# Optimization experiments

Hardware: AMD Instinct MI355X
Metric: run time of the kernel (lower is better)

## Reference

```python
import jax, jax.numpy as jnp
import numpy as np

B, L, S, D, H, CTX = 2, 2048, 512, 1024, 16, 1024
HD = D // H
HID = 4 * D
EPS = 1e-6


def _ln(x):
    mu = jnp.mean(x, axis=-1, keepdims=True)
    var = jnp.mean((x - mu) ** 2, axis=-1, keepdims=True)
    return (x - mu) * jax.lax.rsqrt(var + EPS)


def _rotate_half(x):
    x1, x2 = jnp.split(x, 2, axis=-1)
    return jnp.concatenate([-x2, x1], axis=-1)


def _heads(t):  # [B,N,D] -> [B,H,N,HD]
    return t.reshape(t.shape[0], t.shape[1], H, HD).transpose(0, 2, 1, 3)


def _merge(t):  # [B,H,N,HD] -> [B,N,D]
    return t.transpose(0, 2, 1, 3).reshape(t.shape[0], t.shape[2], D)


def setup_inputs() -> dict:
    key = jax.random.key(0)
    ks = jax.random.split(key, 24)
    s = 0.02
    inp = {
        "x": jax.random.normal(ks[0], (B, L, D), jnp.float32),
        "timestep_emb": jax.random.normal(ks[1], (B, D), jnp.float32),
        "context_emb": jax.random.normal(ks[2], (B, S, CTX), jnp.float32),
        "rope_emb": jax.random.normal(ks[3], (L, HD), jnp.float32),
        # adaLN modulation: Linear(D -> 6D) with bias
        "w_mod": jax.random.normal(ks[4], (D, 6 * D), jnp.float32) * s,
        "b_mod": jnp.zeros((6 * D,), jnp.float32),
        # self-attention (no qkv bias, out has bias)
        "wq_s": jax.random.normal(ks[5], (D, D), jnp.float32) * s,
        "wk_s": jax.random.normal(ks[6], (D, D), jnp.float32) * s,
        "wv_s": jax.random.normal(ks[7], (D, D), jnp.float32) * s,
        "wo_s": jax.random.normal(ks[8], (D, D), jnp.float32) * s,
        "bo_s": jnp.zeros((D,), jnp.float32),
        # cross-attention (q/k/v no bias, out has bias)
        "wq_c": jax.random.normal(ks[9], (D, D), jnp.float32) * s,
        "wk_c": jax.random.normal(ks[10], (CTX, D), jnp.float32) * s,
        "wv_c": jax.random.normal(ks[11], (CTX, D), jnp.float32) * s,
        "wo_c": jax.random.normal(ks[12], (D, D), jnp.float32) * s,
        "bo_c": jnp.zeros((D,), jnp.float32),
        # MLP
        "w1": jax.random.normal(ks[13], (D, HID), jnp.float32) * s,
        "b1": jnp.zeros((HID,), jnp.float32),
        "w2": jax.random.normal(ks[14], (HID, D), jnp.float32) * s,
        "b2": jnp.zeros((D,), jnp.float32),
    }
    return inp


def reference(x, timestep_emb, context_emb, rope_emb,
              w_mod, b_mod,
              wq_s, wk_s, wv_s, wo_s, bo_s,
              wq_c, wk_c, wv_c, wo_c, bo_c,
              w1, b1, w2, b2):
    scale = HD ** -0.5
    # adaLN modulation from timestep embedding
    mods = jnp.split(timestep_emb @ w_mod + b_mod, 6, axis=-1)
    shift_msa, scale_msa, gate_msa, shift_mlp, scale_mlp, gate_mlp = mods

    # --- self-attention with RoPE ---
    nx = _ln(x) * (1.0 + scale_msa[:, None, :]) + shift_msa[:, None, :]
    q = _heads(nx @ wq_s)
    k = _heads(nx @ wk_s)
    v = _heads(nx @ wv_s)
    cos = jnp.cos(rope_emb)[None, None]  # [1,1,L,HD]
    sin = jnp.sin(rope_emb)[None, None]
    q = q * cos + _rotate_half(q) * sin
    k = k * cos + _rotate_half(k) * sin
    attn = jax.nn.softmax(jnp.einsum("bhqd,bhkd->bhqk", q, k) * scale, axis=-1)
    sa = _merge(jnp.einsum("bhqk,bhkd->bhqd", attn, v)) @ wo_s + bo_s
    x = x + gate_msa[:, None, :] * sa

    # --- cross-attention (no mask) ---
    nx = _ln(x)
    q = _heads(nx @ wq_c)
    k = _heads(context_emb @ wk_c)
    v = _heads(context_emb @ wv_c)
    attn = jax.nn.softmax(jnp.einsum("bhqd,bhkd->bhqk", q, k) * scale, axis=-1)
    ca = _merge(jnp.einsum("bhqk,bhkd->bhqd", attn, v)) @ wo_c + bo_c
    x = x + ca

    # --- MLP with modulation + gate ---
    nx = _ln(x) * (1.0 + scale_mlp[:, None, :]) + shift_mlp[:, None, :]
    h = jax.nn.gelu(nx @ w1 + b1, approximate=False)
    x = x + gate_mlp[:, None, :] * (h @ w2 + b2)
    return x
```

## Files before the change

kernel.cpp:

```cpp
#include <hip/hip_runtime.h>
#include <hip/hip_bf16.h>


typedef short short8 __attribute__((ext_vector_type(8)));
typedef float f32x4 __attribute__((ext_vector_type(4)));
typedef float f32x16 __attribute__((ext_vector_type(16)));

#define DEV __device__ __forceinline__

DEV unsigned short f2b(float f) {
  __hip_bfloat16 h = __float2bfloat16(f);
  return *reinterpret_cast<unsigned short*>(&h);
}
DEV float b2f(unsigned short u) {
  unsigned int x = ((unsigned int)u) << 16;
  return __builtin_bit_cast(float, x);
}
DEV unsigned int pk2(float lo, float hi) {
  unsigned int r;
  asm("v_cvt_pk_bf16_f32 %0, %1, %2" : "=v"(r) : "v"(lo), "v"(hi));
  return r;
}
DEV void vpsw(unsigned int& a, unsigned int& b) {
  asm("v_permlane32_swap_b32 %0, %1" : "+v"(a), "+v"(b));
}
DEV float max3f(float a, float b, float c) {
  float r;
  asm("v_max3_f32 %0, %1, %2, %3" : "=v"(r) : "v"(a), "v"(b), "v"(c));
  return r;
}

#define GLB(p) ((const __attribute__((address_space(1))) void*)(p))
#define LDSP(p) ((__attribute__((address_space(3))) void*)(p))

struct TCB { const float* in; unsigned short* out; float scale; };
struct PrepArgs {
  const float* wmod; unsigned short* wmodT;
  TCB sq[8];
  const float* w1; unsigned short* w1T;
  const float* w2; unsigned short* w2T;
  const float* ctx; unsigned short* ctxb;
  const float* rope; float2* cs;
};

__global__ __launch_bounds__(256) void prep(PrepArgs a) {
  __shared__ float t32[32][33];
  const int blk = blockIdx.x;
  const int tx = threadIdx.x & 31, ty = threadIdx.x >> 5;
  if (blk < 22528) {
    const float* in;
    unsigned short* out;
    int R, C, gx, tile;
    float scale;
    if (blk < 6144) {
      in = a.wmod; out = a.wmodT; R = 1024; C = 6144; gx = 192; tile = blk; scale = 1.f;
    } else if (blk < 14336) {
      int j = (blk - 6144) >> 10;
      tile = (blk - 6144) & 1023;
      in = a.sq[j].in; out = a.sq[j].out; scale = a.sq[j].scale;
      R = 1024; C = 1024; gx = 32;
    } else if (blk < 18432) {
      tile = blk - 14336;
      in = a.w1; out = a.w1T; R = 1024; C = 4096; gx = 128; scale = 1.f;
    } else {
      tile = blk - 18432;
      in = a.w2; out = a.w2T; R = 4096; C = 1024; gx = 32; scale = 1.f;
    }
    int bx = (tile % gx) * 32, by = (tile / gx) * 32;
#pragma unroll
    for (int i = ty; i < 32; i += 8)
      t32[i][tx] = in[(size_t)(by + i) * C + bx + tx];
    __syncthreads();
#pragma unroll
    for (int i = ty; i < 32; i += 8)
      out[(size_t)(bx + i) * R + by + tx] = f2b(t32[tx][i] * scale);
  } else if (blk < 26624) {
    int i = (blk - 22528) * 256 + threadIdx.x;
    a.ctxb[i] = f2b(a.ctx[i]);
  } else {
    int i = (blk - 26624) * 256 + threadIdx.x;
    float v = a.rope[i];
    a.cs[i] = make_float2(cosf(v), sinf(v));
  }
}

__global__ __launch_bounds__(256) void mods_kernel(
    const float* __restrict__ te, const unsigned short* __restrict__ wmodT,
    const float* __restrict__ bmod, float* __restrict__ mods) {
  int w = blockIdx.x * 4 + (threadIdx.x >> 6);
  int lane = threadIdx.x & 63;
  int b = w / 6144, j = w % 6144;
  const unsigned short* wr = wmodT + (size_t)j * 1024;
  const float* ter = te + (size_t)b * 1024;
  int k0 = lane * 16;
  float sum = 0.f;
#pragma unroll
  for (int u = 0; u < 2; ++u) {
    short8 wv = *(const short8*)(wr + k0 + u * 8);
#pragma unroll
    for (int e = 0; e < 8; ++e)
      sum += b2f((unsigned short)wv[e]) * ter[k0 + u * 8 + e];
  }
#pragma unroll
  for (int off = 32; off >= 1; off >>= 1) sum += __shfl_down(sum, off);
  if (lane == 0) mods[(size_t)b * 6144 + j] = sum + bmod[j];
}

__global__ __launch_bounds__(256) void ln_mod(
    const float* __restrict__ x, const float* __restrict__ mods,
    unsigned short* __restrict__ out, int scale_ofs, int shift_ofs) {
  int row = blockIdx.x;
  int b = row >> 11;
  int tid = threadIdx.x;
  const float* xr = x + (size_t)row * 1024;
  float4 v = ((const float4*)xr)[tid];
  float s = v.x + v.y + v.z + v.w;
  float ss = v.x * v.x + v.y * v.y + v.z * v.z + v.w * v.w;
#pragma unroll
  for (int off = 32; off >= 1; off >>= 1) {
    s += __shfl_down(s, off);
    ss += __shfl_down(ss, off);
  }
  __shared__ float red[8];
  int wave = tid >> 6, lane = tid & 63;
  if (lane == 0) { red[wave] = s; red[4 + wave] = ss; }
  __syncthreads();
  if (tid == 0) {
    float S = red[0] + red[1] + red[2] + red[3];
    float SS = red[4] + red[5] + red[6] + red[7];
    float mu = S * (1.f / 1024.f);
    red[0] = mu;
    red[1] = SS * (1.f / 1024.f) - mu * mu;
  }
  __syncthreads();
  float mu = red[0];
  float rs = rsqrtf(red[1] + 1e-6f);
  float vv[4] = {v.x, v.y, v.z, v.w};
  unsigned short o[4];
#pragma unroll
  for (int c = 0; c < 4; ++c) {
    int col = tid * 4 + c;
    float nv = (vv[c] - mu) * rs;
    if (scale_ofs >= 0)
      nv = nv * (1.f + mods[(size_t)b * 6144 + scale_ofs + col]) +
           mods[(size_t)b * 6144 + shift_ofs + col];
    o[c] = f2b(nv);
  }
  *(ushort4*)(&out[(size_t)row * 1024 + tid * 4]) = *(const ushort4*)o;
}

template <int EPI, int MI, int NJ>
DEV void gemm_epilogue(f32x4 (&acc)[MI][NJ], void* Cout, const float* bias,
                       const float* mods, int gate_ofs, const float* src,
                       int N, int rowsPerB, int m0, int n0, int wm, int wn,
                       int g, int r) {
#pragma unroll
  for (int i = 0; i < MI; ++i) {
#pragma unroll
    for (int j = 0; j < NJ; ++j) {
#pragma unroll
      for (int q = 0; q < 4; ++q) {
        size_t grow = (size_t)(m0 + wm + i * 16 + g * 4 + q);
        size_t gcol = (size_t)(n0 + wn + j * 16 + r);
        float v = acc[i][j][q];
        if constexpr (EPI == 0) {
          ((unsigned short*)Cout)[grow * N + gcol] = f2b(v);
        } else if constexpr (EPI == 1) {
          v += bias[gcol];
          float ge = 0.5f * v * (1.0f + erff(v * 0.70710678f));
          ((unsigned short*)Cout)[grow * N + gcol] = f2b(ge);
        } else if constexpr (EPI == 3) {
          size_t buf = gcol >> 10;
          ((unsigned short*)Cout)[buf * (4096ull * 1024) + grow * 1024 + (gcol & 1023)] = f2b(v);
        } else {
          v += bias[gcol];
          float gate = 1.0f;
          if (gate_ofs >= 0)
            gate = mods[(grow / rowsPerB) * 6144 + gate_ofs + gcol];
          ((float*)Cout)[grow * N + gcol] = src[grow * N + gcol] + gate * v;
        }
      }
    }
  }
}

DEV void qkv_rope_epilogue(f32x4 (&acc)[4][4], unsigned short* Cout,
                           const float2* cs, int m0, int n0, int wm, int wn,
                           int g, int r) {
  const int buf = (n0 + wn) >> 10;
  const int colbase = (n0 + wn) & 1023;
  unsigned short* base = Cout + (size_t)buf * (4096ull * 1024);
#pragma unroll
  for (int i = 0; i < 4; ++i) {
#pragma unroll
    for (int q = 0; q < 4; ++q) {
      size_t grow = (size_t)(m0 + wm + i * 16 + g * 4 + q);
      unsigned short* orow = base + grow * 1024 + colbase + r;
      if (buf < 2) {
        int l = (int)(grow & 2047);
#pragma unroll
        for (int j = 0; j < 2; ++j) {
          int d = j * 16 + r;
          float2 a = cs[l * 64 + d];
          float2 bb = cs[l * 64 + d + 32];
          float x1 = acc[i][j][q], x2 = acc[i][j + 2][q];
          orow[j * 16] = f2b(x1 * a.x - x2 * a.y);
          orow[(j + 2) * 16] = f2b(x2 * bb.x + x1 * bb.y);
        }
      } else {
#pragma unroll
        for (int j = 0; j < 4; ++j) orow[j * 16] = f2b(acc[i][j][q]);
      }
    }
  }
}

template <int EPI>
__global__ __launch_bounds__(256, 2) void gemm_bt(
    const unsigned short* __restrict__ A, const unsigned short* __restrict__ Bt,
    void* __restrict__ Cout, const float* __restrict__ bias,
    const float* __restrict__ mods, int gate_ofs, const float* __restrict__ src,
    int M, int N, int K, int rowsPerB) {
  __shared__ unsigned short As[128 * 32];
  __shared__ unsigned short Bs[128 * 32];
  const int tid = threadIdx.x;
  const int wave = tid >> 6, lane = tid & 63;
  const int g = lane >> 4, r = lane & 15;
  const int m0 = blockIdx.y * 128, n0 = blockIdx.x * 128;
  const int wm = (wave >> 1) * 64, wn = (wave & 1) * 64;
  const int srow = lane >> 2;
  const int scol = (lane & 3) * 8;

  f32x4 acc[4][4] = {};

  for (int k0 = 0; k0 < K; k0 += 32) {
    __syncthreads();
#pragma unroll
    for (int cc = 0; cc < 4; ++cc) {
      int c = wave * 4 + cc;
      int isB = c >> 3;
      int cl = c & 7;
      int row = cl * 16 + srow;
      const unsigned short* gsrc =
          isB ? (Bt + (size_t)(n0 + row) * K + k0 + scol)
              : (A + (size_t)(m0 + row) * K + k0 + scol);
      unsigned short* ldst = (isB ? Bs : As) + cl * 512;
      __builtin_amdgcn_global_load_lds(GLB(gsrc), LDSP(ldst), 16, 0, 0);
    }
    __syncthreads();

    short8 bfr[4];
#pragma unroll
    for (int j = 0; j < 4; ++j)
      bfr[j] = *(const short8*)(&Bs[(wn + j * 16 + r) * 32 + g * 8]);
#pragma unroll
    for (int i = 0; i < 4; ++i) {
      short8 af = *(const short8*)(&As[(wm + i * 16 + r) * 32 + g * 8]);
#pragma unroll
      for (int j = 0; j < 4; ++j)
        acc[i][j] = __builtin_amdgcn_mfma_f32_16x16x32_bf16(af, bfr[j], acc[i][j], 0, 0, 0);
    }
  }
  gemm_epilogue<EPI, 4, 4>(acc, Cout, bias, mods, gate_ofs, src, N, rowsPerB,
                           m0, n0, wm, wn, g, r);
}

template <int EPI>
__global__ __launch_bounds__(256) void gemm_pipe(
    const unsigned short* __restrict__ A, const unsigned short* __restrict__ Bt,
    void* __restrict__ Cout, const float* __restrict__ bias,
    const float* __restrict__ mods, int gate_ofs, const float* __restrict__ src,
    int M, int N, int K, int rowsPerB, int mshift) {
  __shared__ unsigned short lds[4 * 16384];
  const int tid = threadIdx.x;
  const int wave = tid >> 6, lane = tid & 63;
  const int g = lane >> 4, r = lane & 15;
  const int flat = blockIdx.x;
  const int xcd = flat & 7, idx = flat >> 3;
  const int mt = xcd * (1 << mshift) + (idx & ((1 << mshift) - 1));
  const int nt = idx >> mshift;
  const int m0 = mt * 128, n0 = nt * 128;
  const int wm = (wave >> 1) * 64, wn = (wave & 1) * 64;
  const int srow8 = lane >> 3;
  const int sck = (lane & 7) ^ srow8;

  f32x4 acc[4][4] = {};

  auto stage = [&](int t, int bufi) {
    const int k0 = t * 64;
#pragma unroll
    for (int i = 0; i < 8; ++i) {
      int u = wave * 8 + i;
      int isB = u >> 4;
      int uu = u & 15;
      int rl = uu * 8 + srow8;
      const unsigned short* gsrc =
          (isB ? (Bt + (size_t)(n0 + rl) * K) : (A + (size_t)(m0 + rl) * K)) +
          k0 + sck * 8;
      unsigned short* dst = (unsigned short*)lds + bufi * 16384 + isB * 8192 + uu * 512;
      __builtin_amdgcn_global_load_lds(GLB(gsrc), LDSP(dst), 16, 0, 0);
    }
  };

  const int nt_k = K / 64;
  stage(0, 0);
  stage(1, 1);
  stage(2, 2);

  for (int t = 0; t < nt_k; ++t) {
    int rem = nt_k - t;
    if (rem >= 3) {
      asm volatile("s_waitcnt vmcnt(16)" ::: "memory");
    } else if (rem == 2) {
      asm volatile("s_waitcnt vmcnt(8)" ::: "memory");
    } else {
      asm volatile("s_waitcnt vmcnt(0)" ::: "memory");
    }
    __builtin_amdgcn_sched_barrier(0);
    __builtin_amdgcn_s_barrier();
    __builtin_amdgcn_sched_barrier(0);
    if (t + 3 < nt_k) stage(t + 3, (t + 3) & 3);

    const unsigned short* Ab = (const unsigned short*)lds + (t & 3) * 16384;
    const unsigned short* Bb = Ab + 8192;
#pragma unroll
    for (int ks = 0; ks < 2; ++ks) {
      short8 bfr[4];
#pragma unroll
      for (int j = 0; j < 4; ++j) {
        int row = wn + j * 16 + r;
        bfr[j] = *(const short8*)&Bb[row * 64 + ((g + ks * 4) ^ (r & 7)) * 8];
      }
#pragma unroll
      for (int i = 0; i < 4; ++i) {
        int row = wm + i * 16 + r;
        short8 af = *(const short8*)&Ab[row * 64 + ((g + ks * 4) ^ (r & 7)) * 8];
#pragma unroll
        for (int j = 0; j < 4; ++j)
          acc[i][j] = __builtin_amdgcn_mfma_f32_16x16x32_bf16(af, bfr[j], acc[i][j], 0, 0, 0);
      }
    }
  }
  if constexpr (EPI == 4) {
    qkv_rope_epilogue(acc, (unsigned short*)Cout, (const float2*)bias,
                      m0, n0, wm, wn, g, r);
  } else {
    gemm_epilogue<EPI, 4, 4>(acc, Cout, bias, mods, gate_ofs, src, N, rowsPerB,
                             m0, n0, wm, wn, g, r);
  }
}

template <int EPI>
__global__ __launch_bounds__(256) void gemm_p2(
    const unsigned short* __restrict__ A, const unsigned short* __restrict__ Bt,
    void* __restrict__ Cout, const float* __restrict__ bias,
    const float* __restrict__ mods, int gate_ofs, const float* __restrict__ src,
    int M, int N, int K, int rowsPerB, int ntn) {
  __shared__ unsigned short lds[3 * 12288];
  const int tid = threadIdx.x;
  const int wave = tid >> 6, lane = tid & 63;
  const int g = lane >> 4, r = lane & 15;
  const int flat = blockIdx.x;
  const int nt = flat % ntn, mt = flat / ntn;
  const int m0 = mt * 64, n0 = nt * 128;
  const int wm = (wave >> 1) * 32, wn = (wave & 1) * 64;
  const int srow8 = lane >> 3;
  const int sck = (lane & 7) ^ srow8;

  f32x4 acc[2][4] = {};

  auto stage = [&](int t, int bufi) {
    const int k0 = t * 64;
    unsigned short* base = (unsigned short*)lds + bufi * 12288;
#pragma unroll
    for (int i = 0; i < 2; ++i) {
      int u = wave * 2 + i;
      int rl = u * 8 + srow8;
      const unsigned short* gsrc = A + (size_t)(m0 + rl) * K + k0 + sck * 8;
      __builtin_amdgcn_global_load_lds(GLB(gsrc), LDSP(base + u * 512), 16, 0, 0);
    }
#pragma unroll
    for (int i = 0; i < 4; ++i) {
      int u = wave * 4 + i;
      int rl = u * 8 + srow8;
      const unsigned short* gsrc = Bt + (size_t)(n0 + rl) * K + k0 + sck * 8;
      __builtin_amdgcn_global_load_lds(GLB(gsrc), LDSP(base + 4096 + u * 512), 16, 0, 0);
    }
  };

  const int ntk = K / 64;
  stage(0, 0);
  stage(1, 1);
  int cbuf = 0, sbuf = 2;

  for (int t = 0; t < ntk; ++t) {
    if (t < ntk - 1) {
      asm volatile("s_waitcnt vmcnt(6)" ::: "memory");
    } else {
      asm volatile("s_waitcnt vmcnt(0)" ::: "memory");
    }
    __builtin_amdgcn_sched_barrier(0);
    __builtin_amdgcn_s_barrier();
    __builtin_amdgcn_sched_barrier(0);
    if (t + 2 < ntk) {
      stage(t + 2, sbuf);
      sbuf = (sbuf == 2) ? 0 : sbuf + 1;
    }

    const unsigned short* Ab = (const unsigned short*)lds + cbuf * 12288;
    const unsigned short* Bb = Ab + 4096;
#pragma unroll
    for (int ks = 0; ks < 2; ++ks) {
      short8 bfr[4];
#pragma unroll
      for (int j = 0; j < 4; ++j) {
        int row = wn + j * 16 + r;
        bfr[j] = *(const short8*)&Bb[row * 64 + ((g + ks * 4) ^ (r & 7)) * 8];
      }
#pragma unroll
      for (int i = 0; i < 2; ++i) {
        int row = wm + i * 16 + r;
        short8 af = *(const short8*)&Ab[row * 64 + ((g + ks * 4) ^ (r & 7)) * 8];
#pragma unroll
        for (int j = 0; j < 4; ++j)
          acc[i][j] = __builtin_amdgcn_mfma_f32_16x16x32_bf16(af, bfr[j], acc[i][j], 0, 0, 0);
      }
    }
    cbuf = (cbuf == 2) ? 0 : cbuf + 1;
  }
  gemm_epilogue<EPI, 2, 4>(acc, Cout, bias, mods, gate_ofs, src, N, rowsPerB,
                           m0, n0, wm, wn, g, r);
}

__global__ __launch_bounds__(256) void gemm_cross(
    const unsigned short* __restrict__ Anx, const unsigned short* __restrict__ Bq,
    unsigned short* __restrict__ Oq,
    const unsigned short* __restrict__ Actx, const unsigned short* __restrict__ Bkv,
    unsigned short* __restrict__ Okv) {
  __shared__ unsigned short lds[3 * 12288];
  const int tid = threadIdx.x;
  const int wave = tid >> 6, lane = tid & 63;
  const int g = lane >> 4, r = lane & 15;
  const bool iskv = blockIdx.x >= 512;
  const int flat = iskv ? (blockIdx.x - 512) : blockIdx.x;
  const int ntn = iskv ? 16 : 8;
  const unsigned short* A = iskv ? Actx : Anx;
  const unsigned short* Bt = iskv ? Bkv : Bq;
  const int nt = flat % ntn, mt = flat / ntn;
  const int m0 = mt * 64, n0 = nt * 128;
  const int K = 1024;
  const int wm = (wave >> 1) * 32, wn = (wave & 1) * 64;
  const int srow8 = lane >> 3;
  const int sck = (lane & 7) ^ srow8;

  f32x4 acc[2][4] = {};

  auto stage = [&](int t, int bufi) {
    const int k0 = t * 64;
    unsigned short* base = (unsigned short*)lds + bufi * 12288;
#pragma unroll
    for (int i = 0; i < 2; ++i) {
      int u = wave * 2 + i;
      int rl = u * 8 + srow8;
      const unsigned short* gsrc = A + (size_t)(m0 + rl) * K + k0 + sck * 8;
      __builtin_amdgcn_global_load_lds(GLB(gsrc), LDSP(base + u * 512), 16, 0, 0);
    }
#pragma unroll
    for (int i = 0; i < 4; ++i) {
      int u = wave * 4 + i;
      int rl = u * 8 + srow8;
      const unsigned short* gsrc = Bt + (size_t)(n0 + rl) * K + k0 + sck * 8;
      __builtin_amdgcn_global_load_lds(GLB(gsrc), LDSP(base + 4096 + u * 512), 16, 0, 0);
    }
  };

  const int ntk = K / 64;
  stage(0, 0);
  stage(1, 1);
  int cbuf = 0, sbuf = 2;

  for (int t = 0; t < ntk; ++t) {
    if (t < ntk - 1) {
      asm volatile("s_waitcnt vmcnt(6)" ::: "memory");
    } else {
      asm volatile("s_waitcnt vmcnt(0)" ::: "memory");
    }
    __builtin_amdgcn_sched_barrier(0);
    __builtin_amdgcn_s_barrier();
    __builtin_amdgcn_sched_barrier(0);
    if (t + 2 < ntk) {
      stage(t + 2, sbuf);
      sbuf = (sbuf == 2) ? 0 : sbuf + 1;
    }

    const unsigned short* Ab = (const unsigned short*)lds + cbuf * 12288;
    const unsigned short* Bb = Ab + 4096;
#pragma unroll
    for (int ks = 0; ks < 2; ++ks) {
      short8 bfr[4];
#pragma unroll
      for (int j = 0; j < 4; ++j) {
        int row = wn + j * 16 + r;
        bfr[j] = *(const short8*)&Bb[row * 64 + ((g + ks * 4) ^ (r & 7)) * 8];
      }
#pragma unroll
      for (int i = 0; i < 2; ++i) {
        int row = wm + i * 16 + r;
        short8 af = *(const short8*)&Ab[row * 64 + ((g + ks * 4) ^ (r & 7)) * 8];
#pragma unroll
        for (int j = 0; j < 4; ++j)
          acc[i][j] = __builtin_amdgcn_mfma_f32_16x16x32_bf16(af, bfr[j], acc[i][j], 0, 0, 0);
      }
    }
    cbuf = (cbuf == 2) ? 0 : cbuf + 1;
  }

#pragma unroll
  for (int i = 0; i < 2; ++i) {
#pragma unroll
    for (int j = 0; j < 4; ++j) {
#pragma unroll
      for (int q = 0; q < 4; ++q) {
        size_t grow = (size_t)(m0 + wm + i * 16 + g * 4 + q);
        size_t gcol = (size_t)(n0 + wn + j * 16 + r);
        float v = acc[i][j][q];
        if (iskv) {
          size_t buf = gcol >> 10;
          Okv[buf * (4096ull * 1024) + grow * 1024 + (gcol & 1023)] = f2b(v);
        } else {
          Oq[grow * 1024 + gcol] = f2b(v);
        }
      }
    }
  }
}

__global__ __launch_bounds__(256, 2) void flash2(
    const unsigned short* __restrict__ Q, const unsigned short* __restrict__ Kv,
    const unsigned short* __restrict__ Vv, unsigned short* __restrict__ O,
    int Lk) {
  __shared__ unsigned short lds[20480];
  const int tid = threadIdx.x, wave = tid >> 6, lane = tid & 63;
  const int hi = lane >> 5, lq = lane & 31;
  const int flat = blockIdx.x;
  const int xcd = flat & 7, rr = flat >> 3;
  const int gl = rr >> 4, qt = rr & 15;
  const int g = xcd * 4 + gl;
  const int h = g & 15, b = g >> 4;
  const int Lq = 2048, D = 1024;

  const unsigned short* Qbase =
      Q + ((size_t)b * Lq + qt * 128 + wave * 32 + lq) * D + h * 64;
  const unsigned short* Kbase = Kv + (size_t)b * Lk * D + h * 64;
  const unsigned short* Vbase = Vv + (size_t)b * Lk * D + h * 64;

  short8 qf[4];
#pragma unroll
  for (int kb = 0; kb < 4; ++kb)
    qf[kb] = *(const short8*)(Qbase + kb * 16 + hi * 8);

  const short8 ones = {0x3F80, 0x3F80, 0x3F80, 0x3F80, 0x3F80, 0x3F80, 0x3F80, 0x3F80};
  const f32x16 z16 = {};

  const int kr0 = tid >> 3, kc0 = tid & 7;
  const int kvp = tid >> 3, db = tid & 7;
  const int kch0 = (kc0 ^ (kr0 & 7) ^ (kr0 >> 3)) & 7;
  const int kch1 = kch0 ^ 4;
  const int f0 = (lq & 7) ^ (lq >> 3);
  const int swz0 = f0 << 4, swz1 = swz0 ^ 64;

  int vby[8];
#pragma unroll
  for (int e = 0; e < 8; ++e) {
    int d = db * 8 + e;
    vby[e] = d * 128 + ((kvp * 4) ^ (((e ^ db) & 7) << 4));
  }

  float m_run = -3.0e38f;
  f32x16 o0 = {}, o1 = {}, lacc = {};
  short8 vr0, vr1;
  short8 pbf[4];

  auto stageK = [&](int t, int bi) {
    const unsigned short* s0 = Kbase + (size_t)(t * 64 + kr0) * D + kch0 * 8;
    const unsigned short* s1 = Kbase + (size_t)(t * 64 + kr0 + 32) * D + kch1 * 8;
    __builtin_amdgcn_global_load_lds(GLB(s0), LDSP(&lds[bi * 4096 + wave * 512]), 16, 0, 0);
    __builtin_amdgcn_global_load_lds(GLB(s1), LDSP(&lds[bi * 4096 + 2048 + wave * 512]), 16, 0, 0);
  };
  auto loadV = [&](int t) {
    const unsigned short* v0 = Vbase + (size_t)(t * 64 + 2 * kvp) * D + db * 8;
    vr0 = *(const short8*)v0;
    vr1 = *(const short8*)(v0 + D);
  };
  auto writeV = [&](int t) {
    char* vt = (char*)&lds[12288 + (t & 1) * 4096];
    union { short8 s; unsigned int u[4]; } a, c;
    a.s = vr0; c.s = vr1;
#pragma unroll
    for (int k = 0; k < 4; ++k) {
      *(unsigned int*)(vt + vby[2 * k]) =
          __builtin_amdgcn_perm(c.u[k], a.u[k], 0x05040100u);
      *(unsigned int*)(vt + vby[2 * k + 1]) =
          __builtin_amdgcn_perm(c.u[k], a.u[k], 0x07060302u);
    }
  };
  auto qk = [&](int bi, f32x16& sa0, f32x16& sa1) {
    const unsigned short* K0 = &lds[bi * 4096];
    {
      int lo = hi * 16;
      short8 a0 = *(const short8*)&K0[lq * 64 + ((lo ^ swz0) >> 1)];
      short8 a1 = *(const short8*)&K0[(32 + lq) * 64 + ((lo ^ swz1) >> 1)];
      sa0 = __builtin_amdgcn_mfma_f32_32x32x16_bf16(a0, qf[0], z16, 0, 0, 0);
      sa1 = __builtin_amdgcn_mfma_f32_32x32x16_bf16(a1, qf[0], z16, 0, 0, 0);
    }
#pragma unroll
    for (int ks = 1; ks < 4; ++ks) {
      int lo = ks * 32 + hi * 16;
      short8 a0 = *(const short8*)&K0[lq * 64 + ((lo ^ swz0) >> 1)];
      short8 a1 = *(const short8*)&K0[(32 + lq) * 64 + ((lo ^ swz1) >> 1)];
      sa0 = __builtin_amdgcn_mfma_f32_32x32x16_bf16(a0, qf[ks], sa0, 0, 0, 0);
      sa1 = __builtin_amdgcn_mfma_f32_32x32x16_bf16(a1, qf[ks], sa1, 0, 0, 0);
    }
  };
  auto finish = [&](f32x16& s0a, f32x16& s1a) {
    float tm[8];
#pragma unroll
    for (int i = 0; i < 8; ++i)
      tm[i] = fmaxf(max3f(s0a[i], s0a[i + 8], s1a[i]), s1a[i + 8]);
    float x = max3f(tm[0], tm[1], tm[2]);
    float y = max3f(tm[3], tm[4], tm[5]);
    float pm = fmaxf(max3f(tm[6], tm[7], x), y);
    {
      unsigned int ua = __builtin_bit_cast(unsigned int, pm), ub = ua;
      vpsw(ua, ub);
      pm = fmaxf(__builtin_bit_cast(float, ua), __builtin_bit_cast(float, ub));
    }
    if (__any(pm - m_run > 8.0f)) {
      float mnew = fmaxf(m_run, pm);
      float alpha = exp2f(m_run - mnew);
      lacc[0] *= alpha;
#pragma unroll
      for (int i = 0; i < 16; ++i) { o0[i] *= alpha; o1[i] *= alpha; }
      m_run = mnew;
    }
    float mc = m_run;
#pragma unroll
    for (int i = 0; i < 16; ++i) s0a[i] = exp2f(s0a[i] - mc);
#pragma unroll
    for (int i = 0; i < 16; ++i) s1a[i] = exp2f(s1a[i] - mc);
#pragma unroll
    for (int kb = 0; kb < 4; ++kb) {
      int bb = (kb & 1) * 8;
      float p0, p1, p2, p3, p4, p5, p6, p7;
      if (kb < 2) {
        p0 = s0a[bb + 0]; p1 = s0a[bb + 1]; p2 = s0a[bb + 2]; p3 = s0a[bb + 3];
        p4 = s0a[bb + 4]; p5 = s0a[bb + 5]; p6 = s0a[bb + 6]; p7 = s0a[bb + 7];
      } else {
        p0 = s1a[bb + 0]; p1 = s1a[bb + 1]; p2 = s1a[bb + 2]; p3 = s1a[bb + 3];
        p4 = s1a[bb + 4]; p5 = s1a[bb + 5]; p6 = s1a[bb + 6]; p7 = s1a[bb + 7];
      }
      unsigned int u0 = pk2(p0, p1), u1 = pk2(p2, p3);
      unsigned int u2 = pk2(p4, p5), u3 = pk2(p6, p7);
      vpsw(u0, u2);
      vpsw(u1, u3);
      union { unsigned int u[4]; short8 s; } fr;
      fr.u[0] = u0; fr.u[1] = u1; fr.u[2] = u2; fr.u[3] = u3;
      pbf[kb] = fr.s;
    }
  };
  auto pv = [&](int t) {
    const unsigned short* V0 = &lds[12288 + (t & 1) * 4096];
    __builtin_amdgcn_s_setprio(1);
#pragma unroll
    for (int kb = 0; kb < 4; ++kb) {
      int lo = kb * 32 + hi * 16;
      short8 vf0 = *(const short8*)&V0[lq * 64 + ((lo ^ swz0) >> 1)];
      short8 vf1 = *(const short8*)&V0[(32 + lq) * 64 + ((lo ^ swz1) >> 1)];
      o0 = __builtin_amdgcn_mfma_f32_32x32x16_bf16(vf0, pbf[kb], o0, 0, 0, 0);
      o1 = __builtin_amdgcn_mfma_f32_32x32x16_bf16(vf1, pbf[kb], o1, 0, 0, 0);
      lacc = __builtin_amdgcn_mfma_f32_32x32x16_bf16(ones, pbf[kb], lacc, 0, 0, 0);
    }
    __builtin_amdgcn_s_setprio(0);
  };

  const int nkt = Lk / 64;

  stageK(0, 0);
  loadV(0);
  writeV(0);
  stageK(1, 1);
  __syncthreads();

  f32x16 sA0, sA1, sB0, sB1;
  qk(0, sA0, sA1);

  auto pstep = [&](int t, f32x16& n0, f32x16& n1, f32x16& p0, f32x16& p1) {
    const int tq = t + 1;
    if (tq < nkt) {
      loadV(tq);
      if (tq + 1 < nkt) stageK(tq + 1, (tq + 1) % 3);
      qk(tq % 3, n0, n1);
    }
    finish(p0, p1);
    if (tq < nkt) writeV(tq);
    pv(t);
    __syncthreads();
  };

  for (int t = 0; t < nkt; t += 2) {
    pstep(t, sB0, sB1, sA0, sA1);
    pstep(t + 1, sA0, sA1, sB0, sB1);
  }

  float rl = 1.0f / lacc[0];
  unsigned short* os = &lds[wave * 2048];
#pragma unroll
  for (int t = 0; t < 2; ++t) {
#pragma unroll
    for (int c = 0; c < 4; ++c) {
      int dbase = 32 * t + 8 * c + 4 * hi;
      float v0 = (t ? o1[4 * c + 0] : o0[4 * c + 0]) * rl;
      float v1 = (t ? o1[4 * c + 1] : o0[4 * c + 1]) * rl;
      float v2 = (t ? o1[4 * c + 2] : o0[4 * c + 2]) * rl;
      float v3 = (t ? o1[4 * c + 3] : o0[4 * c + 3]) * rl;
      int by0 = lq * 128 + ((dbase * 2) ^ ((lq & 7) << 4));
      int by1 = lq * 128 + (((dbase + 2) * 2) ^ ((lq & 7) << 4));
      *(unsigned int*)((char*)os + by0) = pk2(v0, v1);
      *(unsigned int*)((char*)os + by1) = pk2(v2, v3);
    }
  }
  int q2 = lane >> 1;
  unsigned short* orow =
      O + ((size_t)b * Lq + qt * 128 + wave * 32 + q2) * D + h * 64;
#pragma unroll
  for (int j = 0; j < 4; ++j) {
    int j2 = (lane & 1) * 4 + j;
    int byr = q2 * 128 + ((j2 * 16) ^ ((q2 & 7) << 4));
    short8 vv = *(const short8*)((char*)os + byr);
    *(short8*)(orow + j2 * 8) = vv;
  }
}

extern "C" void kernel_launch(void* const* d_in, const int* in_sizes, int n_in,
                              void* d_out, int out_size, void* d_ws, size_t ws_size,
                              hipStream_t stream) {
  (void)in_sizes; (void)n_in; (void)out_size; (void)ws_size;
  const float* x_in = (const float*)d_in[0];
  const float* te   = (const float*)d_in[1];
  const float* ctx  = (const float*)d_in[2];
  const float* rope = (const float*)d_in[3];
  const float* wmod = (const float*)d_in[4];
  const float* bmod = (const float*)d_in[5];
  const float* wqs  = (const float*)d_in[6];
  const float* wks  = (const float*)d_in[7];
  const float* wvs  = (const float*)d_in[8];
  const float* wos  = (const float*)d_in[9];
  const float* bos  = (const float*)d_in[10];
  const float* wqc  = (const float*)d_in[11];
  const float* wkc  = (const float*)d_in[12];
  const float* wvc  = (const float*)d_in[13];
  const float* woc  = (const float*)d_in[14];
  const float* boc  = (const float*)d_in[15];
  const float* w1   = (const float*)d_in[16];
  const float* b1   = (const float*)d_in[17];
  const float* w2   = (const float*)d_in[18];
  const float* b2   = (const float*)d_in[19];
  float* out = (float*)d_out;

  char* w = (char*)d_ws;
  size_t o = 0;
  auto alloc = [&](size_t bytes) {
    char* p = w + o;
    o = (o + bytes + 255) & ~(size_t)255;
    return p;
  };
  unsigned short* wmodT = (unsigned short*)alloc(6144ull * 1024 * 2);
  unsigned short* wqsT  = (unsigned short*)alloc(1024ull * 1024 * 2);
  unsigned short* wksT  = (unsigned short*)alloc(1024ull * 1024 * 2);
  unsigned short* wvsT  = (unsigned short*)alloc(1024ull * 1024 * 2);
  unsigned short* wosT  = (unsigned short*)alloc(1024ull * 1024 * 2);
  unsigned short* wqcT  = (unsigned short*)alloc(1024ull * 1024 * 2);
  unsigned short* wkcT  = (unsigned short*)alloc(1024ull * 1024 * 2);
  unsigned short* wvcT  = (unsigned short*)alloc(1024ull * 1024 * 2);
  unsigned short* wocT  = (unsigned short*)alloc(1024ull * 1024 * 2);
  unsigned short* w1T   = (unsigned short*)alloc(4096ull * 1024 * 2);
  unsigned short* w2T   = (unsigned short*)alloc(1024ull * 4096 * 2);
  float* modsb = (float*)alloc(2ull * 6144 * 4);
  float2* csT  = (float2*)alloc(2048ull * 64 * 8);
  unsigned short* nx   = (unsigned short*)alloc(4096ull * 1024 * 2);
  unsigned short* ctxb = (unsigned short*)alloc(1024ull * 1024 * 2);
  unsigned short* qb = (unsigned short*)alloc(4096ull * 1024 * 2);
  unsigned short* kb = (unsigned short*)alloc(4096ull * 1024 * 2);
  unsigned short* vb = (unsigned short*)alloc(4096ull * 1024 * 2);
  unsigned short* ao = (unsigned short*)alloc(4096ull * 1024 * 2);
  float* xw = (float*)alloc(4096ull * 1024 * 4);
  unsigned short* hbuf = qb;

  const float c1 = 0.125f * 1.4426950408889634f;

  PrepArgs pa;
  pa.wmod = wmod; pa.wmodT = wmodT;
  pa.sq[0] = {wqs, wqsT, c1};
  pa.sq[1] = {wks, wksT, 1.0f};
  pa.sq[2] = {wvs, wvsT, 1.0f};
  pa.sq[3] = {wos, wosT, 1.0f};
  pa.sq[4] = {wqc, wqcT, 1.0f};
  pa.sq[5] = {wkc, wkcT, c1};
  pa.sq[6] = {wvc, wvcT, 1.0f};
  pa.sq[7] = {woc, wocT, 1.0f};
  pa.w1 = w1; pa.w1T = w1T;
  pa.w2 = w2; pa.w2T = w2T;
  pa.ctx = ctx; pa.ctxb = ctxb;
  pa.rope = rope; pa.cs = csT;
  prep<<<27136, 256, 0, stream>>>(pa);
  mods_kernel<<<3072, 256, 0, stream>>>(te, wmodT, bmod, modsb);

  ln_mod<<<4096, 256, 0, stream>>>(x_in, modsb, nx, 1024, 0);
  gemm_pipe<4><<<768, 256, 0, stream>>>(nx, wqsT, qb, (const float*)csT, nullptr, -1, nullptr, 4096, 3072, 1024, 2048, 2);
  flash2<<<512, 256, 0, stream>>>(qb, kb, vb, ao, 2048);
  gemm_p2<2><<<512, 256, 0, stream>>>(ao, wosT, xw, bos, modsb, 2048, x_in, 4096, 1024, 1024, 2048, 8);

  ln_mod<<<4096, 256, 0, stream>>>(xw, modsb, nx, -1, -1);
  gemm_cross<<<768, 256, 0, stream>>>(nx, wqcT, qb, ctxb, wkcT, kb);
  flash2<<<512, 256, 0, stream>>>(qb, kb, vb, ao, 512);
  gemm_p2<2><<<512, 256, 0, stream>>>(ao, wocT, xw, boc, modsb, -1, xw, 4096, 1024, 1024, 2048, 8);

  ln_mod<<<4096, 256, 0, stream>>>(xw, modsb, nx, 4096, 3072);
  gemm_bt<1><<<dim3(32, 32), 256, 0, stream>>>(nx, w1T, hbuf, b1, nullptr, -1, nullptr, 4096, 4096, 1024, 2048);
  gemm_p2<2><<<512, 256, 0, stream>>>(hbuf, w2T, out, b2, modsb, 5120, xw, 4096, 1024, 4096, 2048, 8);
}
```

Measured before the change: 386.3 us.

## Fold adaLN modulation GEMV into prep kernel, drop w_mod transpose

Computes the adaLN modulation vector directly from the fp32 w_mod inside the prep kernel. Each of 24 blocks handles 256 output columns with coalesced row reads and timestep embeddings staged in shared memory. This removes the bf16 transpose of the 6144x1024 w_mod, its workspace buffer and the separate mods_kernel launch. The context bf16 conversion is also vectorised to two elements per thread. The trade-off is that only 24 blocks do a serial 1024-step reduction, and that work may become a tail on the prep kernel's critical path.

```diff
diff --git a/kernel.cpp b/kernel.cpp
--- a/kernel.cpp
+++ b/kernel.cpp
@@ -35,7 +35,7 @@
 
 struct TCB { const float* in; unsigned short* out; float scale; };
 struct PrepArgs {
-  const float* wmod; unsigned short* wmodT;
+  const float* wmod; const float* te; const float* bmod; float* mods;
   TCB sq[8];
   const float* w1; unsigned short* w1T;
   const float* w2; unsigned short* w2T;
@@ -45,25 +45,42 @@
 
 __global__ __launch_bounds__(256) void prep(PrepArgs a) {
   __shared__ float t32[32][33];
+  __shared__ float tes[2048];
   const int blk = blockIdx.x;
-  const int tx = threadIdx.x & 31, ty = threadIdx.x >> 5;
-  if (blk < 22528) {
+  const int tid = threadIdx.x;
+  const int tx = tid & 31, ty = tid >> 5;
+  if (blk < 24) {
+    const int j = blk * 256 + tid;
+    for (int u = tid; u < 2048; u += 256) tes[u] = a.te[u];
+    __syncthreads();
+    float a0 = 0.f, b0 = 0.f, a1 = 0.f, b1 = 0.f;
+#pragma unroll 8
+    for (int k = 0; k < 1024; k += 2) {
+      float v0 = a.wmod[(size_t)k * 6144 + j];
+      float v1 = a.wmod[(size_t)(k + 1) * 6144 + j];
+      a0 += tes[k] * v0;
+      b0 += tes[k + 1] * v1;
+      a1 += tes[1024 + k] * v0;
+      b1 += tes[1024 + k + 1] * v1;
+    }
+    float bm = a.bmod[j];
+    a.mods[j] = a0 + b0 + bm;
+    a.mods[6144 + j] = a1 + b1 + bm;
+  } else if (blk < 16408) {
     const float* in;
     unsigned short* out;
     int R, C, gx, tile;
     float scale;
-    if (blk < 6144) {
-      in = a.wmod; out = a.wmodT; R = 1024; C = 6144; gx = 192; tile = blk; scale = 1.f;
-    } else if (blk < 14336) {
-      int j = (blk - 6144) >> 10;
-      tile = (blk - 6144) & 1023;
+    if (blk < 8216) {
+      int j = (blk - 24) >> 10;
+      tile = (blk - 24) & 1023;
       in = a.sq[j].in; out = a.sq[j].out; scale = a.sq[j].scale;
       R = 1024; C = 1024; gx = 32;
-    } else if (blk < 18432) {
-      tile = blk - 14336;
+    } else if (blk < 12312) {
+      tile = blk - 8216;
       in = a.w1; out = a.w1T; R = 1024; C = 4096; gx = 128; scale = 1.f;
     } else {
-      tile = blk - 18432;
+      tile = blk - 12312;
       in = a.w2; out = a.w2T; R = 4096; C = 1024; gx = 32; scale = 1.f;
     }
     int bx = (tile % gx) * 32, by = (tile / gx) * 32;
@@ -74,36 +91,15 @@
 #pragma unroll
     for (int i = ty; i < 32; i += 8)
       out[(size_t)(bx + i) * R + by + tx] = f2b(t32[tx][i] * scale);
-  } else if (blk < 26624) {
-    int i = (blk - 22528) * 256 + threadIdx.x;
-    a.ctxb[i] = f2b(a.ctx[i]);
+  } else if (blk < 18456) {
+    int i = (blk - 16408) * 512 + tid * 2;
+    float2 v = *(const float2*)&a.ctx[i];
+    *(unsigned int*)&a.ctxb[i] = pk2(v.x, v.y);
   } else {
-    int i = (blk - 26624) * 256 + threadIdx.x;
+    int i = (blk - 18456) * 256 + tid;
     float v = a.rope[i];
     a.cs[i] = make_float2(cosf(v), sinf(v));
   }
-}
-
-__global__ __launch_bounds__(256) void mods_kernel(
-    const float* __restrict__ te, const unsigned short* __restrict__ wmodT,
-    const float* __restrict__ bmod, float* __restrict__ mods) {
-  int w = blockIdx.x * 4 + (threadIdx.x >> 6);
-  int lane = threadIdx.x & 63;
-  int b = w / 6144, j = w % 6144;
-  const unsigned short* wr = wmodT + (size_t)j * 1024;
-  const float* ter = te + (size_t)b * 1024;
-  int k0 = lane * 16;
-  float sum = 0.f;
-#pragma unroll
-  for (int u = 0; u < 2; ++u) {
-    short8 wv = *(const short8*)(wr + k0 + u * 8);
-#pragma unroll
-    for (int e = 0; e < 8; ++e)
-      sum += b2f((unsigned short)wv[e]) * ter[k0 + u * 8 + e];
-  }
-#pragma unroll
-  for (int off = 32; off >= 1; off >>= 1) sum += __shfl_down(sum, off);
-  if (lane == 0) mods[(size_t)b * 6144 + j] = sum + bmod[j];
 }
 
 __global__ __launch_bounds__(256) void ln_mod(
@@ -774,7 +770,6 @@
     o = (o + bytes + 255) & ~(size_t)255;
     return p;
   };
-  unsigned short* wmodT = (unsigned short*)alloc(6144ull * 1024 * 2);
   unsigned short* wqsT  = (unsigned short*)alloc(1024ull * 1024 * 2);
   unsigned short* wksT  = (unsigned short*)alloc(1024ull * 1024 * 2);
   unsigned short* wvsT  = (unsigned short*)alloc(1024ull * 1024 * 2);
@@ -799,7 +794,7 @@
   const float c1 = 0.125f * 1.4426950408889634f;
 
   PrepArgs pa;
-  pa.wmod = wmod; pa.wmodT = wmodT;
+  pa.wmod = wmod; pa.te = te; pa.bmod = bmod; pa.mods = modsb;
   pa.sq[0] = {wqs, wqsT, c1};
   pa.sq[1] = {wks, wksT, 1.0f};
   pa.sq[2] = {wvs, wvsT, 1.0f};
@@ -812,8 +807,7 @@
   pa.w2 = w2; pa.w2T = w2T;
   pa.ctx = ctx; pa.ctxb = ctxb;
   pa.rope = rope; pa.cs = csT;
-  prep<<<27136, 256, 0, stream>>>(pa);
-  mods_kernel<<<3072, 256, 0, stream>>>(te, wmodT, bmod, modsb);
+  prep<<<18968, 256, 0, stream>>>(pa);
 
   ln_mod<<<4096, 256, 0, stream>>>(x_in, modsb, nx, 1024, 0);
   gemm_pipe<4><<<768, 256, 0, stream>>>(nx, wqsT, qb, (const float*)csT, nullptr, -1, nullptr, 4096, 3072, 1024, 2048, 2);
```

Measured after the change: 387.7 us (median of 2 runs). No clear change (+0.4%).
